# Optimization experiments

Measured on AMD Instinct MI355X. Metric: run time of the kernel, lower is better.

Reference implementation:

```python
import jax, jax.numpy as jnp
import numpy as np

HEADS = 2
BN_EPS = 1e-5


def _axial_self_attn(x, Wq, Wkv, Wout, bout):
    # x: (b, s, t, c) -- attend along t (the axial sequence dim)
    b, s, t, c = x.shape
    dh = c // HEADS
    q = (x @ Wq).reshape(b, s, t, HEADS, dh)
    k, v = jnp.split(x @ Wkv, 2, axis=-1)  # matches torch .chunk(2, dim=-1)
    k = k.reshape(b, s, t, HEADS, dh)
    v = v.reshape(b, s, t, HEADS, dh)
    dots = jnp.einsum('bsind,bsjnd->bsnij', q, k) * (dh ** -0.5)
    attn = jax.nn.softmax(dots, axis=-1)
    out = jnp.einsum('bsnij,bsjnd->bsind', attn, v).reshape(b, s, t, c)
    return out @ Wout + bout


def setup_inputs() -> dict:
    key = jax.random.key(0)
    ks = jax.random.split(key, 8)
    B, C, H, W = 8, 128, 256, 256
    E = 2 * C
    sd = 0.05
    return {
        'x': jax.random.normal(ks[0], (B, C, H, W), jnp.float32),
        'Wq_h': jax.random.normal(ks[1], (C, C), jnp.float32) * sd,
        'Wkv_h': jax.random.normal(ks[2], (C, 2 * C), jnp.float32) * sd,
        'Wout_h': jax.random.normal(ks[3], (C, C), jnp.float32) * sd,
        'bout_h': jnp.zeros((C,), jnp.float32),
        'Wq_w': jax.random.normal(ks[4], (C, C), jnp.float32) * sd,
        'Wkv_w': jax.random.normal(ks[5], (C, 2 * C), jnp.float32) * sd,
        'Wout_w': jax.random.normal(ks[6], (C, C), jnp.float32) * sd,
        'bout_w': jnp.zeros((C,), jnp.float32),
        'conv_w': jax.random.normal(ks[7], (E, E), jnp.float32) * sd,  # (in, out); torch conv weight[o,i,0,0].T
        'gamma': jnp.ones((E,), jnp.float32),
        'beta': jnp.zeros((E,), jnp.float32),
    }


def reference(x, Wq_h, Wkv_h, Wout_h, bout_h, Wq_w, Wkv_w, Wout_w, bout_w, conv_w, gamma, beta):
    B, C, H, W = x.shape
    # MaxPool2d(2)
    xp = x.reshape(B, C, H // 2, 2, W // 2, 2).max(axis=(3, 5))  # (B,C,H2,W2)
    xc = jnp.transpose(xp, (0, 2, 3, 1))  # (B,H2,W2,C) channels-last
    # AxialAttention, sum_axial_out=True: height-axis attn + width-axis attn
    a_h = _axial_self_attn(jnp.transpose(xc, (0, 2, 1, 3)), Wq_h, Wkv_h, Wout_h, bout_h)
    a_h = jnp.transpose(a_h, (0, 2, 1, 3))
    a_w = _axial_self_attn(xc, Wq_w, Wkv_w, Wout_w, bout_w)
    a = jax.nn.relu(a_h + a_w)
    # cat((x_attn, x), dim=channel) then conv1x1 -> relu -> BatchNorm (batch stats)
    y = jnp.concatenate([a, xc], axis=-1) @ conv_w  # (B,H2,W2,2C)
    y = jax.nn.relu(y)
    mean = y.mean(axis=(0, 1, 2))
    var = y.var(axis=(0, 1, 2))
    y = (y - mean) * jax.lax.rsqrt(var + BN_EPS) * gamma + beta
    return jnp.transpose(y, (0, 3, 1, 2))  # back to NCHW
```

## Files before the change

kernel.cpp:

```cpp
#include <hip/hip_runtime.h>


typedef short v8s __attribute__((ext_vector_type(8)));
typedef short v4s __attribute__((ext_vector_type(4)));
typedef float v4f __attribute__((ext_vector_type(4)));
typedef float v4flt __attribute__((ext_vector_type(4)));

#define LSA 136
#define LSC 264
#define LSP 130

static __device__ __forceinline__ short f2bf(float f){
  unsigned u = __builtin_bit_cast(unsigned, f);
  u = (u + 0x7FFFu + ((u >> 16) & 1u)) >> 16;
  return (short)u;
}
static __device__ __forceinline__ float bf2f(short s){
  unsigned u = ((unsigned)(unsigned short)s) << 16;
  return __builtin_bit_cast(float, u);
}

__global__ void prep_kernel(const float* __restrict__ Wq_h, const float* __restrict__ Wkv_h,
                            const float* __restrict__ Wout_h, const float* __restrict__ Wq_w,
                            const float* __restrict__ Wkv_w, const float* __restrict__ Wout_w,
                            const float* __restrict__ conv_w, short* __restrict__ wt,
                            float* __restrict__ stats){
  int idx = blockIdx.x * 256 + threadIdx.x;
  if (idx < 8192) stats[idx] = 0.0f;
  const float* src; int K, O, base;
  if      (idx <  16384){ base = 0;      K=128; O=128; src=Wq_h;  }
  else if (idx <  49152){ base = 16384;  K=128; O=256; src=Wkv_h; }
  else if (idx <  65536){ base = 49152;  K=128; O=128; src=Wout_h;}
  else if (idx <  81920){ base = 65536;  K=128; O=128; src=Wq_w;  }
  else if (idx < 114688){ base = 81920;  K=128; O=256; src=Wkv_w; }
  else if (idx < 131072){ base = 114688; K=128; O=128; src=Wout_w;}
  else                  { base = 131072; K=256; O=256; src=conv_w;}
  int local = idx - base;
  int o = local / K, i = local - o * K;
  wt[idx] = f2bf(src[i * O + o]);
}

__global__ __launch_bounds__(256, 4)
void pool_kernel(const float* __restrict__ x, short* __restrict__ xp){
  __shared__ short t_[128*LSP];
  int bx = blockIdx.x;
  int b = bx >> 7, i = bx & 127;
  int tid = (int)threadIdx.x;
  int j2 = tid & 63;
  int cq = tid >> 6;
  for (int rep = 0; rep < 32; ++rep){
    int c = cq*32 + rep;
    const float* p0 = x + (((b*128 + c)*256 + 2*i)*256 + 4*j2);
    v4flt a  = *(const v4flt*)p0;
    v4flt bb = *(const v4flt*)(p0 + 256);
    t_[(2*j2)*LSP + c]   = f2bf(fmaxf(fmaxf(a[0], a[1]), fmaxf(bb[0], bb[1])));
    t_[(2*j2+1)*LSP + c] = f2bf(fmaxf(fmaxf(a[2], a[3]), fmaxf(bb[2], bb[3])));
  }
  __syncthreads();
  int obase = ((b*128 + i)*128)*128;
  for (int rep = 0; rep < 8; ++rep){
    int idx = rep*256 + tid;
    int row = idx >> 4, seg = idx & 15;
    *(v8s*)(xp + obase + row*128 + seg*8) = *(const v8s*)(&t_[row*LSP + seg*8]);
  }
}

__global__ __launch_bounds__(512, 6)
void attn_kernel(const short* __restrict__ xp, const short* __restrict__ wt,
                 const float* __restrict__ bout_h, const float* __restrict__ bout_w,
                 short* __restrict__ ah, short* __restrict__ aw){
  __shared__ short A[128*LSA];
  __shared__ short WB[64*LSA];

  const int bx = blockIdx.x;
  const int dir = bx & 1;
  const int sb = bx >> 1;
  const int b = sb >> 7, s = sb & 127;
  const int tid = (int)threadIdx.x;
  const int w = tid >> 6;
  const int lane = tid & 63;
  const int l15 = lane & 15, l4 = lane >> 4;

  const short* Wq   = wt + dir*65536;
  const short* Wk   = Wq + 16384;
  const short* Wv   = Wq + 32768;
  const short* Wout = Wq + 49152;
  const float* bsrc = dir ? bout_w : bout_h;
  short*       ao   = dir ? aw : ah;

  const int trow = 16*w + l15;
  const int xbase = dir ? (((b*128 + s)*128 + trow)*128)
                        : (((b*128 + trow)*128 + s)*128);
  v8s av[4];
  #pragma unroll
  for (int kk = 0; kk < 4; ++kk)
    av[kk] = *(const v8s*)(xp + xbase + kk*32 + l4*8);

#define STAGE_H(SRC, HF)                                                 \
  { _Pragma("unroll")                                                    \
    for (int r_ = 0; r_ < 2; ++r_){                                      \
      int idx_ = r_*512 + tid;                              \
      int oc_ = idx_ >> 4, seg_ = idx_ & 15;                             \
      *(v8s*)(&WB[oc_*LSA + seg_*8]) =                                   \
          *(const v8s*)((SRC) + (64*(HF) + oc_)*128 + seg_*8);           \
    } }

#define QK_HALF(HF)                                                      \
  { _Pragma("unroll")                                                    \
    for (int tcl = 0; tcl < 4; ++tcl){                                   \
      int tc = 4*(HF) + tcl;                                             \
      v4f d = {0.f,0.f,0.f,0.f};                                         \
      _Pragma("unroll")                                                  \
      for (int kk = 0; kk < 4; ++kk){                                    \
        v8s bf = *(const v8s*)(&WB[(tcl*16 + l15)*LSA + kk*32 + l4*8]);  \
        d = __builtin_amdgcn_mfma_f32_16x16x32_bf16(av[kk], bf, d, 0, 0, 0); \
      }                                                                  \
      _Pragma("unroll")                                                  \
      for (int r = 0; r < 4; ++r)                                        \
        A[(16*w + 4*l4 + r)*LSA + 16*tc + l15] = f2bf(d[r]);             \
    } }

  STAGE_H(Wq, 0); __syncthreads();
  QK_HALF(0);     __syncthreads();
  STAGE_H(Wq, 1); __syncthreads();
  QK_HALF(1);
  v8s bq[2][2];
  #pragma unroll
  for (int h = 0; h < 2; ++h)
    #pragma unroll
    for (int kk = 0; kk < 2; ++kk)
      bq[h][kk] = *(const v8s*)(&A[(16*w + l15)*LSA + h*64 + kk*32 + l4*8]);
  __syncthreads();

  STAGE_H(Wk, 0); __syncthreads();
  QK_HALF(0);     __syncthreads();
  STAGE_H(Wk, 1); __syncthreads();
  QK_HALF(1);     __syncthreads();

  STAGE_H(Wv, 0);

  v4s pk[2][8];
  #pragma unroll
  for (int h = 0; h < 2; ++h){
    v4f st[8];
    #pragma unroll
    for (int jt = 0; jt < 8; ++jt){
      v4f d = {0.f,0.f,0.f,0.f};
      #pragma unroll
      for (int kk = 0; kk < 2; ++kk){
        v8s ak = *(const v8s*)(&A[(16*jt + l15)*LSA + h*64 + kk*32 + l4*8]);
        d = __builtin_amdgcn_mfma_f32_16x16x32_bf16(ak, bq[h][kk], d, 0, 0, 0);
      }
      st[jt] = d;
    }
    float mx = -1e30f;
    #pragma unroll
    for (int jt = 0; jt < 8; ++jt)
      #pragma unroll
      for (int r = 0; r < 4; ++r) mx = fmaxf(mx, st[jt][r]);
    mx = fmaxf(mx, __shfl_xor(mx, 16));
    mx = fmaxf(mx, __shfl_xor(mx, 32));
    float sm = 0.f;
    #pragma unroll
    for (int jt = 0; jt < 8; ++jt)
      #pragma unroll
      for (int r = 0; r < 4; ++r){
        float e = __expf((st[jt][r] - mx) * 0.125f);
        st[jt][r] = e; sm += e;
      }
    sm += __shfl_xor(sm, 16);
    sm += __shfl_xor(sm, 32);
    float inv = 1.0f / sm;
    #pragma unroll
    for (int jt = 0; jt < 8; ++jt)
      #pragma unroll
      for (int r = 0; r < 4; ++r) pk[h][jt][r] = f2bf(st[jt][r] * inv);
  }
  __syncthreads();

  v8s pa[2][4];
  #pragma unroll
  for (int h = 0; h < 2; ++h){
    #pragma unroll
    for (int jt = 0; jt < 8; ++jt)
      *(v4s*)(&A[(16*w + l15)*LSA + 16*jt + 4*l4]) = pk[h][jt];
    #pragma unroll
    for (int kk = 0; kk < 4; ++kk)
      pa[h][kk] = *(const v8s*)(&A[(16*w + l15)*LSA + kk*32 + l4*8]);
  }
  __syncthreads();

  #pragma unroll
  for (int tcl = 0; tcl < 4; ++tcl){
    int tc = tcl;
    v4f d = {0.f,0.f,0.f,0.f};
    #pragma unroll
    for (int kk = 0; kk < 4; ++kk){
      v8s bf = *(const v8s*)(&WB[(tcl*16 + l15)*LSA + kk*32 + l4*8]);
      d = __builtin_amdgcn_mfma_f32_16x16x32_bf16(av[kk], bf, d, 0, 0, 0);
    }
    v4s pkv;
    #pragma unroll
    for (int r = 0; r < 4; ++r) pkv[r] = f2bf(d[r]);
    *(v4s*)(&A[(16*tc + l15)*LSA + 16*w + 4*l4]) = pkv;
  }
  __syncthreads();
  STAGE_H(Wv, 1); __syncthreads();
  #pragma unroll
  for (int tcl = 0; tcl < 4; ++tcl){
    int tc = 4 + tcl;
    v4f d = {0.f,0.f,0.f,0.f};
    #pragma unroll
    for (int kk = 0; kk < 4; ++kk){
      v8s bf = *(const v8s*)(&WB[(tcl*16 + l15)*LSA + kk*32 + l4*8]);
      d = __builtin_amdgcn_mfma_f32_16x16x32_bf16(av[kk], bf, d, 0, 0, 0);
    }
    v4s pkv;
    #pragma unroll
    for (int r = 0; r < 4; ++r) pkv[r] = f2bf(d[r]);
    *(v4s*)(&A[(16*tc + l15)*LSA + 16*w + 4*l4]) = pkv;
  }
  __syncthreads();

  STAGE_H(Wout, 0);

  v4f ot[2][4];
  #pragma unroll
  for (int h = 0; h < 2; ++h)
    #pragma unroll
    for (int tc = 0; tc < 4; ++tc){
      v4f d = {0.f,0.f,0.f,0.f};
      #pragma unroll
      for (int kk = 0; kk < 4; ++kk){
        v8s vf = *(const v8s*)(&A[(64*h + 16*tc + l15)*LSA + kk*32 + l4*8]);
        d = __builtin_amdgcn_mfma_f32_16x16x32_bf16(vf, pa[h][kk], d, 0, 0, 0);
      }
      ot[h][tc] = d;
    }
  __syncthreads();

  #pragma unroll
  for (int h = 0; h < 2; ++h)
    #pragma unroll
    for (int tc = 0; tc < 4; ++tc){
      v4s pko;
      #pragma unroll
      for (int r = 0; r < 4; ++r) pko[r] = f2bf(ot[h][tc][r]);
      *(v4s*)(&A[(16*w + l15)*LSA + 64*h + 16*tc + 4*l4]) = pko;
    }
  v8s ob[4];
  #pragma unroll
  for (int kk = 0; kk < 4; ++kk)
    ob[kk] = *(const v8s*)(&A[(16*w + l15)*LSA + kk*32 + l4*8]);

#define OUTPROJ_HALF(HF)                                                 \
  { _Pragma("unroll")                                                    \
    for (int tcl = 0; tcl < 4; ++tcl){                                   \
      int tc = 4*(HF) + tcl;                                             \
      v4f d = {0.f,0.f,0.f,0.f};                                         \
      _Pragma("unroll")                                                  \
      for (int kk = 0; kk < 4; ++kk){                                    \
        v8s awf = *(const v8s*)(&WB[(tcl*16 + l15)*LSA + kk*32 + l4*8]); \
        d = __builtin_amdgcn_mfma_f32_16x16x32_bf16(awf, ob[kk], d, 0, 0, 0); \
      }                                                                  \
      v4f bias = *(const v4f*)(bsrc + 16*tc + 4*l4);                     \
      v4s z;                                                             \
      _Pragma("unroll")                                                  \
      for (int r = 0; r < 4; ++r) z[r] = f2bf(d[r] + bias[r]);           \
      *(v4s*)(&A[(16*w + l15)*LSA + 16*tc + 4*l4]) = z;                  \
    } }

  OUTPROJ_HALF(0);
  __syncthreads();
  STAGE_H(Wout, 1); __syncthreads();
  OUTPROJ_HALF(1);
  __syncthreads();

  int obase = ((b*128 + s)*128)*128;
  #pragma unroll
  for (int r = 0; r < 4; ++r){
    int idx = (r*512 + tid) * 8;
    int t = idx >> 7, c = idx & 127;
    *(v8s*)(ao + obase + t*128 + c) = *(const v8s*)(&A[t*LSA + c]);
  }
#undef STAGE_H
#undef QK_HALF
#undef OUTPROJ_HALF
}

__global__ __launch_bounds__(512, 2)
void conv_kernel(const short* __restrict__ ah, const short* __restrict__ aw,
                 const short* __restrict__ xp, const short* __restrict__ wt,
                 short* __restrict__ yb, float* __restrict__ stats){
  __shared__ short cats[128*LSC];
  __shared__ float lsum[256];
  __shared__ float lsq[256];
  const short* convT = wt + 131072;
  int bx = blockIdx.x;
  int b = bx >> 7, ii = bx & 127;
  int tid = (int)threadIdx.x;
  int wv = tid >> 6, lane = tid & 63, l15 = lane & 15, l4 = lane >> 4;
  if (tid < 256){ lsum[tid] = 0.f; lsq[tid] = 0.f; }

  v8s wf[2][8];
  #pragma unroll
  for (int x = 0; x < 2; ++x)
    #pragma unroll
    for (int kk = 0; kk < 8; ++kk)
      wf[x][kk] = *(const v8s*)(convT + (((wv + 8*x)*16 + l15)*256) + kk*32 + l4*8);

  for (int r = 0; r < 4; ++r){
    int idx = (r*512 + tid) * 8;
    int t = idx >> 7, c = idx & 127;
    v8s hv = *(const v8s*)(ah + ((b*128 + t)*128 + ii)*128 + c);
    v8s wv_ = *(const v8s*)(aw + ((b*128 + ii)*128 + t)*128 + c);
    v8s o;
    #pragma unroll
    for (int k = 0; k < 8; ++k)
      o[k] = f2bf(fmaxf(bf2f(hv[k]) + bf2f(wv_[k]), 0.f));
    *(v8s*)(&cats[t*LSC + c]) = o;
    *(v8s*)(&cats[t*LSC + 128 + c]) =
        *(const v8s*)(xp + ((b*128 + ii)*128 + t)*128 + c);
  }
  __syncthreads();

  v4s ypk[2][8];
  float s1[2] = {0.f,0.f}, s2[2] = {0.f,0.f};
  #pragma unroll
  for (int tt = 0; tt < 8; ++tt){
    v4f d0 = {0.f,0.f,0.f,0.f}, d1 = {0.f,0.f,0.f,0.f};
    #pragma unroll
    for (int kk = 0; kk < 8; ++kk){
      v8s af = *(const v8s*)(&cats[(16*tt + l15)*LSC + kk*32 + l4*8]);
      d0 = __builtin_amdgcn_mfma_f32_16x16x32_bf16(af, wf[0][kk], d0, 0, 0, 0);
      d1 = __builtin_amdgcn_mfma_f32_16x16x32_bf16(af, wf[1][kk], d1, 0, 0, 0);
    }
    #pragma unroll
    for (int r = 0; r < 4; ++r){
      float y0 = fmaxf(d0[r], 0.f), y1 = fmaxf(d1[r], 0.f);
      ypk[0][tt][r] = f2bf(y0); ypk[1][tt][r] = f2bf(y1);
      s1[0] += y0; s2[0] += y0*y0;
      s1[1] += y1; s2[1] += y1*y1;
    }
  }
  #pragma unroll
  for (int x = 0; x < 2; ++x){
    s1[x] += __shfl_xor(s1[x], 16); s1[x] += __shfl_xor(s1[x], 32);
    s2[x] += __shfl_xor(s2[x], 16); s2[x] += __shfl_xor(s2[x], 32);
  }
  if (l4 == 0){
    #pragma unroll
    for (int x = 0; x < 2; ++x){
      int e = (wv + 8*x)*16 + l15;
      atomicAdd(&lsum[e], s1[x]);
      atomicAdd(&lsq[e],  s2[x]);
    }
  }
  __syncthreads();
  #pragma unroll
  for (int x = 0; x < 2; ++x)
    #pragma unroll
    for (int tt = 0; tt < 8; ++tt)
      *(v4s*)(&cats[((wv + 8*x)*16 + l15)*132 + 16*tt + 4*l4]) = ypk[x][tt];
  __syncthreads();
  for (int r = 0; r < 8; ++r){
    int idx = (r*512 + tid) * 8;
    int e = idx >> 7, j = idx & 127;
    *(v8s*)(yb + ((b*256 + e)*128 + ii)*128 + j) = *(const v8s*)(&cats[e*132 + j]);
  }
  if (tid < 256){
    int c = bx & 15;
    atomicAdd(&stats[c*512 + tid],       lsum[tid]);
    atomicAdd(&stats[c*512 + 256 + tid], lsq[tid]);
  }
}

__global__ void bn_kernel(const short* __restrict__ yb, float* __restrict__ out,
                          const float* __restrict__ stats,
                          const float* __restrict__ gamma, const float* __restrict__ beta){
  const float invn = 1.0f / 131072.0f;
  int bx = blockIdx.x;
  int e = bx & 255;
  float s1 = 0.f, s2 = 0.f;
  #pragma unroll
  for (int c = 0; c < 16; ++c){
    s1 += stats[c*512 + e];
    s2 += stats[c*512 + 256 + e];
  }
  float m   = s1 * invn;
  float var = s2 * invn - m * m;
  float sc  = gamma[e] * rsqrtf(var + 1e-5f);
  float sh  = beta[e] - m * sc;
  int base = bx * 16384;
  int tid = (int)threadIdx.x;
  for (int rep = 0; rep < 8; ++rep){
    int idx = base + (rep*256 + tid)*8;
    v8s yv = *(const v8s*)(yb + idx);
    v4f o1, o2;
    #pragma unroll
    for (int r = 0; r < 4; ++r){
      o1[r] = bf2f(yv[r])   * sc + sh;
      o2[r] = bf2f(yv[4+r]) * sc + sh;
    }
    *(v4f*)(out + idx)     = o1;
    *(v4f*)(out + idx + 4) = o2;
  }
}

extern "C" void kernel_launch(void* const* d_in, const int* in_sizes, int n_in,
                              void* d_out, int out_size, void* d_ws, size_t ws_size,
                              hipStream_t stream){
  const float* x      = (const float*)d_in[0];
  const float* Wq_h   = (const float*)d_in[1];
  const float* Wkv_h  = (const float*)d_in[2];
  const float* Wout_h = (const float*)d_in[3];
  const float* bout_h = (const float*)d_in[4];
  const float* Wq_w   = (const float*)d_in[5];
  const float* Wkv_w  = (const float*)d_in[6];
  const float* Wout_w = (const float*)d_in[7];
  const float* bout_w = (const float*)d_in[8];
  const float* conv_w = (const float*)d_in[9];
  const float* gamma  = (const float*)d_in[10];
  const float* beta   = (const float*)d_in[11];
  float* out = (float*)d_out;

  char* ws = (char*)d_ws;
  short* xp    = (short*)(ws);
  short* ah    = (short*)(ws +  33554432);
  short* aw    = (short*)(ws +  67108864);
  short* yb    = (short*)(ws + 100663296);
  short* wt    = (short*)(ws + 167772160);
  float* stats = (float*)(ws + 168165376);

  prep_kernel<<<768, 256, 0, stream>>>(Wq_h, Wkv_h, Wout_h, Wq_w, Wkv_w, Wout_w,
                                       conv_w, wt, stats);
  pool_kernel<<<1024, 256, 0, stream>>>(x, xp);
  attn_kernel<<<2048, 512, 0, stream>>>(xp, wt, bout_h, bout_w, ah, aw);
  conv_kernel<<<1024, 512, 0, stream>>>(ah, aw, xp, wt, yb, stats);
  bn_kernel<<<2048, 256, 0, stream>>>(yb, out, stats, gamma, beta);
}
```

Measured before the change: 274.3 us.

## Prefetch attention weight halves into registers; split conv kernel rows in half

In the attention kernel, each weight half is now loaded from global memory into registers before the preceding MFMA phase runs, and written to shared memory afterwards. This overlaps global load latency with compute instead of stalling on it before each stage. The conv kernel now handles half a row per block, using a smaller shared buffer, twice as many blocks and a launch bound of 4 blocks per CU, to raise occupancy. The cost is extra registers held for the prefetched weights, and each conv block reloads the full conv weights for only half the work.

```diff
diff --git a/kernel.cpp b/kernel.cpp
--- a/kernel.cpp
+++ b/kernel.cpp
@@ -8,6 +8,7 @@
 
 #define LSA 136
 #define LSC 264
+#define LSY 72
 #define LSP 130
 
 static __device__ __forceinline__ short f2bf(float f){
@@ -96,14 +97,13 @@
   for (int kk = 0; kk < 4; ++kk)
     av[kk] = *(const v8s*)(xp + xbase + kk*32 + l4*8);
 
-#define STAGE_H(SRC, HF)                                                 \
-  { _Pragma("unroll")                                                    \
-    for (int r_ = 0; r_ < 2; ++r_){                                      \
-      int idx_ = r_*512 + tid;                              \
-      int oc_ = idx_ >> 4, seg_ = idx_ & 15;                             \
-      *(v8s*)(&WB[oc_*LSA + seg_*8]) =                                   \
-          *(const v8s*)((SRC) + (64*(HF) + oc_)*128 + seg_*8);           \
-    } }
+  v8s rw0, rw1;
+#define LOAD_H(SRC, HF)                                                  \
+  { rw0 = *(const v8s*)((SRC) + (64*(HF) + (tid>>4))*128 + (tid&15)*8);  \
+    rw1 = *(const v8s*)((SRC) + (64*(HF) + 32 + (tid>>4))*128 + (tid&15)*8); }
+#define WRITE_H()                                                        \
+  { *(v8s*)(&WB[(tid>>4)*LSA + (tid&15)*8]) = rw0;                       \
+    *(v8s*)(&WB[(32 + (tid>>4))*LSA + (tid&15)*8]) = rw1; }
 
 #define QK_HALF(HF)                                                      \
   { _Pragma("unroll")                                                    \
@@ -120,9 +120,45 @@
         A[(16*w + 4*l4 + r)*LSA + 16*tc + l15] = f2bf(d[r]);             \
     } }
 
-  STAGE_H(Wq, 0); __syncthreads();
-  QK_HALF(0);     __syncthreads();
-  STAGE_H(Wq, 1); __syncthreads();
+#define V_HALF(HF)                                                       \
+  { _Pragma("unroll")                                                    \
+    for (int tcl = 0; tcl < 4; ++tcl){                                   \
+      int tc = 4*(HF) + tcl;                                             \
+      v4f d = {0.f,0.f,0.f,0.f};                                         \
+      _Pragma("unroll")                                                  \
+      for (int kk = 0; kk < 4; ++kk){                                    \
+        v8s bf = *(const v8s*)(&WB[(tcl*16 + l15)*LSA + kk*32 + l4*8]);  \
+        d = __builtin_amdgcn_mfma_f32_16x16x32_bf16(av[kk], bf, d, 0, 0, 0); \
+      }                                                                  \
+      v4s pkv;                                                           \
+      _Pragma("unroll")                                                  \
+      for (int r = 0; r < 4; ++r) pkv[r] = f2bf(d[r]);                   \
+      *(v4s*)(&A[(16*tc + l15)*LSA + 16*w + 4*l4]) = pkv;                \
+    } }
+
+#define OUTPROJ_HALF(HF)                                                 \
+  { _Pragma("unroll")                                                    \
+    for (int tcl = 0; tcl < 4; ++tcl){                                   \
+      int tc = 4*(HF) + tcl;                                             \
+      v4f d = {0.f,0.f,0.f,0.f};                                         \
+      _Pragma("unroll")                                                  \
+      for (int kk = 0; kk < 4; ++kk){                                    \
+        v8s awf = *(const v8s*)(&WB[(tcl*16 + l15)*LSA + kk*32 + l4*8]); \
+        d = __builtin_amdgcn_mfma_f32_16x16x32_bf16(awf, ob[kk], d, 0, 0, 0); \
+      }                                                                  \
+      v4f bias = *(const v4f*)(bsrc + 16*tc + 4*l4);                     \
+      v4s z;                                                             \
+      _Pragma("unroll")                                                  \
+      for (int r = 0; r < 4; ++r) z[r] = f2bf(d[r] + bias[r]);           \
+      *(v4s*)(&A[(16*w + l15)*LSA + 16*tc + 4*l4]) = z;                  \
+    } }
+
+  LOAD_H(Wq, 0);
+  WRITE_H(); __syncthreads();
+  LOAD_H(Wq, 1);
+  QK_HALF(0); __syncthreads();
+  WRITE_H(); __syncthreads();
+  LOAD_H(Wk, 0);
   QK_HALF(1);
   v8s bq[2][2];
   #pragma unroll
@@ -132,12 +168,13 @@
       bq[h][kk] = *(const v8s*)(&A[(16*w + l15)*LSA + h*64 + kk*32 + l4*8]);
   __syncthreads();
 
-  STAGE_H(Wk, 0); __syncthreads();
-  QK_HALF(0);     __syncthreads();
-  STAGE_H(Wk, 1); __syncthreads();
-  QK_HALF(1);     __syncthreads();
-
-  STAGE_H(Wv, 0);
+  WRITE_H(); __syncthreads();
+  LOAD_H(Wk, 1);
+  QK_HALF(0); __syncthreads();
+  WRITE_H(); __syncthreads();
+  LOAD_H(Wv, 0);
+  QK_HALF(1); __syncthreads();
+  WRITE_H();
 
   v4s pk[2][8];
   #pragma unroll
@@ -190,39 +227,12 @@
   }
   __syncthreads();
 
-  #pragma unroll
-  for (int tcl = 0; tcl < 4; ++tcl){
-    int tc = tcl;
-    v4f d = {0.f,0.f,0.f,0.f};
-    #pragma unroll
-    for (int kk = 0; kk < 4; ++kk){
-      v8s bf = *(const v8s*)(&WB[(tcl*16 + l15)*LSA + kk*32 + l4*8]);
-      d = __builtin_amdgcn_mfma_f32_16x16x32_bf16(av[kk], bf, d, 0, 0, 0);
-    }
-    v4s pkv;
-    #pragma unroll
-    for (int r = 0; r < 4; ++r) pkv[r] = f2bf(d[r]);
-    *(v4s*)(&A[(16*tc + l15)*LSA + 16*w + 4*l4]) = pkv;
-  }
-  __syncthreads();
-  STAGE_H(Wv, 1); __syncthreads();
-  #pragma unroll
-  for (int tcl = 0; tcl < 4; ++tcl){
-    int tc = 4 + tcl;
-    v4f d = {0.f,0.f,0.f,0.f};
-    #pragma unroll
-    for (int kk = 0; kk < 4; ++kk){
-      v8s bf = *(const v8s*)(&WB[(tcl*16 + l15)*LSA + kk*32 + l4*8]);
-      d = __builtin_amdgcn_mfma_f32_16x16x32_bf16(av[kk], bf, d, 0, 0, 0);
-    }
-    v4s pkv;
-    #pragma unroll
-    for (int r = 0; r < 4; ++r) pkv[r] = f2bf(d[r]);
-    *(v4s*)(&A[(16*tc + l15)*LSA + 16*w + 4*l4]) = pkv;
-  }
-  __syncthreads();
-
-  STAGE_H(Wout, 0);
+  LOAD_H(Wv, 1);
+  V_HALF(0); __syncthreads();
+  WRITE_H(); __syncthreads();
+  LOAD_H(Wout, 0);
+  V_HALF(1); __syncthreads();
+  WRITE_H();
 
   v4f ot[2][4];
   #pragma unroll
@@ -252,27 +262,10 @@
   #pragma unroll
   for (int kk = 0; kk < 4; ++kk)
     ob[kk] = *(const v8s*)(&A[(16*w + l15)*LSA + kk*32 + l4*8]);
-
-#define OUTPROJ_HALF(HF)                                                 \
-  { _Pragma("unroll")                                                    \
-    for (int tcl = 0; tcl < 4; ++tcl){                                   \
-      int tc = 4*(HF) + tcl;                                             \
-      v4f d = {0.f,0.f,0.f,0.f};                                         \
-      _Pragma("unroll")                                                  \
-      for (int kk = 0; kk < 4; ++kk){                                    \
-        v8s awf = *(const v8s*)(&WB[(tcl*16 + l15)*LSA + kk*32 + l4*8]); \
-        d = __builtin_amdgcn_mfma_f32_16x16x32_bf16(awf, ob[kk], d, 0, 0, 0); \
-      }                                                                  \
-      v4f bias = *(const v4f*)(bsrc + 16*tc + 4*l4);                     \
-      v4s z;                                                             \
-      _Pragma("unroll")                                                  \
-      for (int r = 0; r < 4; ++r) z[r] = f2bf(d[r] + bias[r]);           \
-      *(v4s*)(&A[(16*w + l15)*LSA + 16*tc + 4*l4]) = z;                  \
-    } }
-
+  LOAD_H(Wout, 1);
   OUTPROJ_HALF(0);
   __syncthreads();
-  STAGE_H(Wout, 1); __syncthreads();
+  WRITE_H(); __syncthreads();
   OUTPROJ_HALF(1);
   __syncthreads();
 
@@ -283,21 +276,25 @@
     int t = idx >> 7, c = idx & 127;
     *(v8s*)(ao + obase + t*128 + c) = *(const v8s*)(&A[t*LSA + c]);
   }
-#undef STAGE_H
+#undef LOAD_H
+#undef WRITE_H
 #undef QK_HALF
+#undef V_HALF
 #undef OUTPROJ_HALF
 }
 
-__global__ __launch_bounds__(512, 2)
+__global__ __launch_bounds__(512, 4)
 void conv_kernel(const short* __restrict__ ah, const short* __restrict__ aw,
                  const short* __restrict__ xp, const short* __restrict__ wt,
                  short* __restrict__ yb, float* __restrict__ stats){
-  __shared__ short cats[128*LSC];
+  __shared__ short cats[256*LSY];
   __shared__ float lsum[256];
   __shared__ float lsq[256];
   const short* convT = wt + 131072;
   int bx = blockIdx.x;
-  int b = bx >> 7, ii = bx & 127;
+  int half = bx & 1;
+  int row = bx >> 1;
+  int b = row >> 7, ii = row & 127;
   int tid = (int)threadIdx.x;
   int wv = tid >> 6, lane = tid & 63, l15 = lane & 15, l4 = lane >> 4;
   if (tid < 256){ lsum[tid] = 0.f; lsq[tid] = 0.f; }
@@ -309,25 +306,27 @@
     for (int kk = 0; kk < 8; ++kk)
       wf[x][kk] = *(const v8s*)(convT + (((wv + 8*x)*16 + l15)*256) + kk*32 + l4*8);
 
-  for (int r = 0; r < 4; ++r){
+  #pragma unroll
+  for (int r = 0; r < 2; ++r){
     int idx = (r*512 + tid) * 8;
     int t = idx >> 7, c = idx & 127;
-    v8s hv = *(const v8s*)(ah + ((b*128 + t)*128 + ii)*128 + c);
-    v8s wv_ = *(const v8s*)(aw + ((b*128 + ii)*128 + t)*128 + c);
+    int tg = 64*half + t;
+    v8s hv = *(const v8s*)(ah + ((b*128 + tg)*128 + ii)*128 + c);
+    v8s wv_ = *(const v8s*)(aw + ((b*128 + ii)*128 + tg)*128 + c);
     v8s o;
     #pragma unroll
     for (int k = 0; k < 8; ++k)
       o[k] = f2bf(fmaxf(bf2f(hv[k]) + bf2f(wv_[k]), 0.f));
     *(v8s*)(&cats[t*LSC + c]) = o;
     *(v8s*)(&cats[t*LSC + 128 + c]) =
-        *(const v8s*)(xp + ((b*128 + ii)*128 + t)*128 + c);
-  }
-  __syncthreads();
-
-  v4s ypk[2][8];
+        *(const v8s*)(xp + ((b*128 + ii)*128 + tg)*128 + c);
+  }
+  __syncthreads();
+
+  v4s ypk[2][4];
   float s1[2] = {0.f,0.f}, s2[2] = {0.f,0.f};
   #pragma unroll
-  for (int tt = 0; tt < 8; ++tt){
+  for (int tt = 0; tt < 4; ++tt){
     v4f d0 = {0.f,0.f,0.f,0.f}, d1 = {0.f,0.f,0.f,0.f};
     #pragma unroll
     for (int kk = 0; kk < 8; ++kk){
@@ -360,13 +359,15 @@
   #pragma unroll
   for (int x = 0; x < 2; ++x)
     #pragma unroll
-    for (int tt = 0; tt < 8; ++tt)
-      *(v4s*)(&cats[((wv + 8*x)*16 + l15)*132 + 16*tt + 4*l4]) = ypk[x][tt];
-  __syncthreads();
-  for (int r = 0; r < 8; ++r){
-    int idx = (r*512 + tid) * 8;
-    int e = idx >> 7, j = idx & 127;
-    *(v8s*)(yb + ((b*256 + e)*128 + ii)*128 + j) = *(const v8s*)(&cats[e*132 + j]);
+    for (int tt = 0; tt < 4; ++tt)
+      *(v4s*)(&cats[((wv + 8*x)*16 + l15)*LSY + 16*tt + 4*l4]) = ypk[x][tt];
+  __syncthreads();
+  #pragma unroll
+  for (int r = 0; r < 4; ++r){
+    int idxv = r*512 + tid;
+    int e = idxv >> 3, jseg = idxv & 7;
+    *(v8s*)(yb + ((b*256 + e)*128 + ii)*128 + 64*half + jseg*8) =
+        *(const v8s*)(&cats[e*LSY + jseg*8]);
   }
   if (tid < 256){
     int c = bx & 15;
@@ -436,6 +437,6 @@
                                        conv_w, wt, stats);
   pool_kernel<<<1024, 256, 0, stream>>>(x, xp);
   attn_kernel<<<2048, 512, 0, stream>>>(xp, wt, bout_h, bout_w, ah, aw);
-  conv_kernel<<<1024, 512, 0, stream>>>(ah, aw, xp, wt, yb, stats);
+  conv_kernel<<<2048, 512, 0, stream>>>(ah, aw, xp, wt, yb, stats);
   bn_kernel<<<2048, 256, 0, stream>>>(yb, out, stats, gamma, beta);
 }
```

New measurement: 264.8 us. -3.5%, faster.
